# Kernel optimization log

Measured on AMD Instinct MI355X. Metric: run time of the kernel, lower is better.

Reference implementation:

```python
import jax, jax.numpy as jnp
import numpy as np

B, C, H, W = 2, 1024, 64, 64
R, E, HE, T, K = 16, 4, 512, 3, 2


def setup_inputs() -> dict:
    key = jax.random.key(0)
    ks = jax.random.split(key, 12)
    s = 0.02
    return {
        "x": jax.random.normal(ks[0], (B, C, H, W), jnp.float32),
        "t": jax.random.normal(ks[1], (B, C, H, W), jnp.float32),
        "fc_w": jax.random.normal(ks[2], (C, 2 * C), jnp.float32) * s,
        "ln_g": jnp.ones((C,), jnp.float32),
        "ln_b": jnp.zeros((C,), jnp.float32),
        "f1_w1": jax.random.normal(ks[3], (C // R, C), jnp.float32) * s,
        "f1_b1": jnp.zeros((C // R,), jnp.float32),
        "f1_wa": jax.random.normal(ks[4], (C, C // R), jnp.float32) * s,
        "f1_ba": jnp.zeros((C,), jnp.float32),
        "f1_wb": jax.random.normal(ks[5], (C, C // R), jnp.float32) * s,
        "f1_bb": jnp.zeros((C,), jnp.float32),
        "w_gate": jax.random.normal(ks[6], (T, C, E), jnp.float32) * s,
        "e_w1": jax.random.normal(ks[7], (E, C, HE), jnp.float32) * s,
        "e_b1": jnp.zeros((E, HE), jnp.float32),
        "e_w2": jax.random.normal(ks[8], (E, HE, C), jnp.float32) * s,
        "e_b2": jnp.zeros((E, C), jnp.float32),
        "task_index": 1,
    }


def _cv_squared(v):
    eps = 1e-10
    return jnp.var(v, ddof=1) / (jnp.mean(v) ** 2 + eps)


def reference(x, t, fc_w, ln_g, ln_b, f1_w1, f1_b1, f1_wa, f1_ba, f1_wb, f1_bb,
              w_gate, e_w1, e_b1, e_w2, e_b2, task_index):
    b, c, h, w = x.shape
    n = h * w
    # MultiTaskGeneralFusion: SE-style dual-branch channel gating
    s = jnp.mean(x + t, axis=(2, 3))                        # [B, C]
    hid = jax.nn.relu(s @ f1_w1.T + f1_b1)                  # [B, C/r]
    a = hid @ f1_wa.T + f1_ba                               # [B, C]
    bb = hid @ f1_wb.T + f1_bb                              # [B, C]
    wts = jax.nn.softmax(jnp.stack([a, bb], axis=0), axis=0)  # [2, B, C]
    z = wts[0][:, :, None, None] * x + wts[1][:, :, None, None] * t
    # fused linear -> ReLU -> LayerNorm on concatenated tokens
    x3 = x.reshape(b, c, n).transpose(0, 2, 1)              # [B, N, C]
    t3 = t.reshape(b, c, n).transpose(0, 2, 1)
    y = jnp.concatenate([x3, t3], axis=-1)                  # [B, N, 2C]
    y = jax.nn.relu(jnp.einsum('bnd,cd->bnc', y, fc_w))     # [B, N, C]
    mu = jnp.mean(y, axis=-1, keepdims=True)
    var = jnp.mean((y - mu) ** 2, axis=-1, keepdims=True)
    y = (y - mu) * jax.lax.rsqrt(var + 1e-5) * ln_g + ln_b
    yf = y.reshape(b * n, c)                                # [BN, C]
    # MMoE top-k gating (eval mode: no gating noise)
    logits = yf @ w_gate[task_index]                        # [BN, E]
    top_logits, top_idx = jax.lax.top_k(logits, K)          # [BN, K]
    top_gates = jax.nn.softmax(top_logits, axis=-1)
    gates = jnp.zeros_like(logits).at[jnp.arange(b * n)[:, None], top_idx].set(top_gates)
    # dense expert compute, gated combine
    eh = jax.nn.relu(jnp.einsum('nc,ech->neh', yf, e_w1) + e_b1)   # [BN, E, HE]
    eo = jnp.einsum('neh,eho->neo', eh, e_w2) + e_b2               # [BN, E, C]
    ym = jnp.einsum('ne,neo->no', gates, eo)                        # [BN, C]
    importance = gates.sum(axis=0)
    load = (gates > 0).sum(axis=0).astype(jnp.float32)
    aux_loss = _cv_squared(importance) + _cv_squared(load)
    y4 = ym.reshape(b, n, c).transpose(0, 2, 1).reshape(b, c, h, w) + z
    return (y4, aux_loss)
```

## Files before the change

kernel.cpp:

```cpp
#include <hip/hip_runtime.h>
#include <cstddef>
#include <cstdint>

#define B_   2
#define C_   1024
#define N_   4096
#define M_   8192
#define K2_  2048
#define E_   4
#define HE_  512

typedef float f32x4 __attribute__((ext_vector_type(4)));
typedef short bf16x8 __attribute__((ext_vector_type(8)));
typedef _Float16 f16x8 __attribute__((ext_vector_type(8)));
typedef unsigned short u16x8 __attribute__((ext_vector_type(8)));

static __device__ __forceinline__ unsigned short f2bf(float f) {
  unsigned int u = __float_as_uint(f);
  u = u + 0x7fffu + ((u >> 16) & 1u);
  return (unsigned short)(u >> 16);
}

static __device__ __forceinline__ void gl_lds16(const void* g, void* l) {
  __builtin_amdgcn_global_load_lds(
      (const __attribute__((address_space(1))) void*)(uintptr_t)g,
      (__attribute__((address_space(3))) void*)(unsigned)(uintptr_t)l,
      16, 0, 0);
}

static __device__ __forceinline__ bf16x8 cvt8(f32x4 a, f32x4 b) {
  union { unsigned u[4]; bf16x8 s; } r;
  asm("v_cvt_pk_bf16_f32 %0, %1, %2" : "=v"(r.u[0]) : "v"(a[0]), "v"(a[1]));
  asm("v_cvt_pk_bf16_f32 %0, %1, %2" : "=v"(r.u[1]) : "v"(a[2]), "v"(a[3]));
  asm("v_cvt_pk_bf16_f32 %0, %1, %2" : "=v"(r.u[2]) : "v"(b[0]), "v"(b[1]));
  asm("v_cvt_pk_bf16_f32 %0, %1, %2" : "=v"(r.u[3]) : "v"(b[2]), "v"(b[3]));
  return r.s;
}

__global__ __launch_bounds__(256) void k_reduce_s(const float* __restrict__ x,
                                                  const float* __restrict__ t,
                                                  float* __restrict__ s) {
  const int bc = blockIdx.x;
  const float* xp = x + (size_t)bc * N_;
  const float* tp = t + (size_t)bc * N_;
  float acc = 0.f;
  for (int i = threadIdx.x; i < N_ / 4; i += 256) {
    const float4 a = ((const float4*)xp)[i];
    const float4 b = ((const float4*)tp)[i];
    acc += ((a.x + b.x) + (a.y + b.y)) + ((a.z + b.z) + (a.w + b.w));
  }
  #pragma unroll
  for (int o = 32; o; o >>= 1) acc += __shfl_down(acc, o);
  __shared__ float red[4];
  if ((threadIdx.x & 63) == 0) red[threadIdx.x >> 6] = acc;
  __syncthreads();
  if (threadIdx.x == 0)
    s[bc] = (red[0] + red[1] + red[2] + red[3]) * (1.f / (float)N_);
}

__global__ __launch_bounds__(256) void k_se_gate(const float* __restrict__ s,
                                                 const float* __restrict__ w1, const float* __restrict__ b1,
                                                 const float* __restrict__ wa, const float* __restrict__ ba,
                                                 const float* __restrict__ wb, const float* __restrict__ bbv,
                                                 float* __restrict__ wts0) {
  __shared__ float hid[2][64];
  const int t = threadIdx.x;
  if (t < 128) {
    const int b = t >> 6, r = t & 63;
    float acc = b1[r];
    const float* sp = s + b * C_;
    const float* wp = w1 + r * C_;
    for (int c = 0; c < C_; ++c) acc = fmaf(sp[c], wp[c], acc);
    hid[b][r] = fmaxf(acc, 0.f);
  }
  __syncthreads();
  for (int o = t; o < B_ * C_; o += 256) {
    const int b = o >> 10, c = o & 1023;
    float a = ba[c], bb = bbv[c];
    #pragma unroll 8
    for (int r = 0; r < 64; ++r) {
      const float h = hid[b][r];
      a  = fmaf(h, wa[c * 64 + r], a);
      bb = fmaf(h, wb[c * 64 + r], bb);
    }
    wts0[o] = 1.f / (1.f + expf(bb - a));
  }
}

__global__ __launch_bounds__(256) void k_prep_act(const float* __restrict__ xb,
                                                  const float* __restrict__ tb,
                                                  _Float16* __restrict__ ah,
                                                  _Float16* __restrict__ am) {
  __shared__ float tile[64][65];
  const int c0 = blockIdx.x * 64, n0 = blockIdx.y * 64;
  const int tid = threadIdx.x;
  #pragma unroll
  for (int srcsel = 0; srcsel < 2; ++srcsel) {
    const float* src = srcsel ? tb : xb;
    const int koff = srcsel ? C_ : 0;
    if (srcsel) __syncthreads();
    #pragma unroll
    for (int p = 0; p < 4; ++p) {
      const int f = tid + p * 256;
      const int cr = f >> 4, nq = f & 15;
      const float4 v = *(const float4*)(src + (size_t)(c0 + cr) * N_ + n0 + nq * 4);
      tile[cr][nq * 4 + 0] = v.x; tile[cr][nq * 4 + 1] = v.y;
      tile[cr][nq * 4 + 2] = v.z; tile[cr][nq * 4 + 3] = v.w;
    }
    __syncthreads();
    #pragma unroll
    for (int p = 0; p < 2; ++p) {
      const int f = tid + p * 256;
      const int mr = f >> 3, kq = f & 7;
      f16x8 hv, mv;
      #pragma unroll
      for (int u = 0; u < 8; ++u) {
        const float v = tile[kq * 8 + u][mr] * 64.f;
        const _Float16 h = (_Float16)v;
        hv[u] = h;
        mv[u] = (_Float16)(v - (float)h);
      }
      const size_t off = (size_t)(n0 + mr) * K2_ + koff + c0 + kq * 8;
      *(f16x8*)(ah + off) = hv;
      *(f16x8*)(am + off) = mv;
    }
  }
}

__global__ __launch_bounds__(256) void k_prep_fcw(const float* __restrict__ w,
                                                  _Float16* __restrict__ wh,
                                                  _Float16* __restrict__ wm) {
  const size_t i = ((size_t)blockIdx.x * 256 + threadIdx.x) * 8;
  const float4 v0 = *(const float4*)(w + i);
  const float4 v1 = *(const float4*)(w + i + 4);
  const float vv[8] = {v0.x, v0.y, v0.z, v0.w, v1.x, v1.y, v1.z, v1.w};
  f16x8 hv, mv;
  #pragma unroll
  for (int u = 0; u < 8; ++u) {
    const float sv = vv[u] * 4096.f;
    const _Float16 h = (_Float16)sv;
    hv[u] = h;
    mv[u] = (_Float16)(sv - (float)h);
  }
  *(f16x8*)(wh + i) = hv;
  *(f16x8*)(wm + i) = mv;
}

__global__ __launch_bounds__(256) void k_prep_tr(const float* __restrict__ src, long long zs, int srs,
                                                 unsigned short* __restrict__ dst, long long zo, int drs) {
  __shared__ float tile[64][65];
  const int c0 = blockIdx.x * 64, r0 = blockIdx.y * 64, z = blockIdx.z;
  const float* s = src + (size_t)z * zs;
  unsigned short* d = dst + (size_t)z * zo;
  const int tid = threadIdx.x;
  #pragma unroll
  for (int p = 0; p < 4; ++p) {
    const int f = tid + p * 256;
    const int rr = f >> 4, cq = f & 15;
    const float4 v = *(const float4*)(s + (size_t)(r0 + rr) * srs + c0 + cq * 4);
    tile[rr][cq * 4 + 0] = v.x; tile[rr][cq * 4 + 1] = v.y;
    tile[rr][cq * 4 + 2] = v.z; tile[rr][cq * 4 + 3] = v.w;
  }
  __syncthreads();
  #pragma unroll
  for (int p = 0; p < 2; ++p) {
    const int f = tid + p * 256;
    const int cr = f >> 3, rq = f & 7;
    u16x8 o;
    #pragma unroll
    for (int u = 0; u < 8; ++u) o[u] = f2bf(tile[rq * 8 + u][cr]);
    *(u16x8*)(d + (size_t)(c0 + cr) * drs + r0 + rq * 8) = o;
  }
}

__global__ __launch_bounds__(256) void k_fc_mfma(const _Float16* __restrict__ Ah,
                                                 const _Float16* __restrict__ Am,
                                                 const _Float16* __restrict__ Bh,
                                                 const _Float16* __restrict__ Bm,
                                                 float* __restrict__ y) {
  __shared__ __align__(16) _Float16 lAh[4096], lAm[4096], lBh[4096], lBm[4096];
  const int tid = threadIdx.x, w = tid >> 6, l = tid & 63;
  const int m0 = blockIdx.y * 128, n0 = blockIdx.x * 128;
  const int wr = w >> 1, wc = w & 1, lg = l >> 4, lr = l & 15;
  f32x4 acc[4][4] = {};
  for (int k0 = 0; k0 < K2_; k0 += 32) {
    #pragma unroll
    for (int p = 0; p < 2; ++p) {
      const int c = w * 2 + p;
      const int i = c * 64 + l;
      const int g = i >> 7, row = i & 127;
      const size_t ga = (size_t)(m0 + row) * K2_ + k0 + g * 8;
      const size_t gb = (size_t)(n0 + row) * K2_ + k0 + g * 8;
      gl_lds16(Ah + ga, (char*)lAh + c * 1024);
      gl_lds16(Am + ga, (char*)lAm + c * 1024);
      gl_lds16(Bh + gb, (char*)lBh + c * 1024);
      gl_lds16(Bm + gb, (char*)lBm + c * 1024);
    }
    __syncthreads();
    f16x8 ah[4], am[4], bh[4], bm[4];
    #pragma unroll
    for (int i = 0; i < 4; ++i) {
      const int off = (lg * 128 + wr * 64 + i * 16 + lr) * 8;
      ah[i] = *(const f16x8*)&lAh[off];
      am[i] = *(const f16x8*)&lAm[off];
    }
    #pragma unroll
    for (int j = 0; j < 4; ++j) {
      const int off = (lg * 128 + wc * 64 + j * 16 + lr) * 8;
      bh[j] = *(const f16x8*)&lBh[off];
      bm[j] = *(const f16x8*)&lBm[off];
    }
    #pragma unroll
    for (int i = 0; i < 4; ++i)
      #pragma unroll
      for (int j = 0; j < 4; ++j) {
        acc[i][j] = __builtin_amdgcn_mfma_f32_16x16x32_f16(ah[i], bh[j], acc[i][j], 0, 0, 0);
        acc[i][j] = __builtin_amdgcn_mfma_f32_16x16x32_f16(ah[i], bm[j], acc[i][j], 0, 0, 0);
        acc[i][j] = __builtin_amdgcn_mfma_f32_16x16x32_f16(am[i], bh[j], acc[i][j], 0, 0, 0);
      }
    __syncthreads();
  }
  #pragma unroll
  for (int i = 0; i < 4; ++i) {
    const int mb = m0 + wr * 64 + i * 16 + lg * 4;
    #pragma unroll
    for (int j = 0; j < 4; ++j) {
      const int n = n0 + wc * 64 + j * 16 + lr;
      #pragma unroll
      for (int r = 0; r < 4; ++r)
        y[(size_t)(mb + r) * C_ + n] = fmaxf(acc[i][j][r] * (1.f / 262144.f), 0.f);
    }
  }
}

__global__ __launch_bounds__(256) void k_ln_topk(float* __restrict__ y,
                                                 const float* __restrict__ lng, const float* __restrict__ lnb,
                                                 const float* __restrict__ wg, const int* __restrict__ taskp,
                                                 float* __restrict__ gates) {
  const int wv = threadIdx.x >> 6, ln = threadIdx.x & 63;
  const int m = blockIdx.x * 4 + wv;
  float* yr = y + (size_t)m * C_;
  float4 v[4];
  #pragma unroll
  for (int ch = 0; ch < 4; ++ch) v[ch] = *(const float4*)(yr + ch * 256 + ln * 4);
  float sum = 0.f;
  #pragma unroll
  for (int ch = 0; ch < 4; ++ch) sum += (v[ch].x + v[ch].y) + (v[ch].z + v[ch].w);
  #pragma unroll
  for (int o = 32; o; o >>= 1) sum += __shfl_down(sum, o);
  sum = __shfl(sum, 0);
  const float mu = sum * (1.f / 1024.f);
  float q = 0.f;
  #pragma unroll
  for (int ch = 0; ch < 4; ++ch) {
    const float dx = v[ch].x - mu, dy = v[ch].y - mu, dz = v[ch].z - mu, dw = v[ch].w - mu;
    q += (dx * dx + dy * dy) + (dz * dz + dw * dw);
  }
  #pragma unroll
  for (int o = 32; o; o >>= 1) q += __shfl_down(q, o);
  q = __shfl(q, 0);
  const float rstd = rsqrtf(q * (1.f / 1024.f) + 1e-5f);
  const float* wrow = wg + (size_t)(*taskp) * (C_ * E_);
  float l0 = 0.f, l1 = 0.f, l2 = 0.f, l3 = 0.f;
  #pragma unroll
  for (int ch = 0; ch < 4; ++ch) {
    const int c = ch * 256 + ln * 4;
    const float4 gg = *(const float4*)(lng + c);
    const float4 bv = *(const float4*)(lnb + c);
    float f[4];
    f[0] = (v[ch].x - mu) * rstd * gg.x + bv.x;
    f[1] = (v[ch].y - mu) * rstd * gg.y + bv.y;
    f[2] = (v[ch].z - mu) * rstd * gg.z + bv.z;
    f[3] = (v[ch].w - mu) * rstd * gg.w + bv.w;
    float4 wb; wb.x = f[0]; wb.y = f[1]; wb.z = f[2]; wb.w = f[3];
    *(float4*)(yr + c) = wb;
    #pragma unroll
    for (int i = 0; i < 4; ++i) {
      const float4 we = *(const float4*)(wrow + (size_t)(c + i) * 4);
      l0 = fmaf(f[i], we.x, l0); l1 = fmaf(f[i], we.y, l1);
      l2 = fmaf(f[i], we.z, l2); l3 = fmaf(f[i], we.w, l3);
    }
  }
  #pragma unroll
  for (int o = 32; o; o >>= 1) {
    l0 += __shfl_down(l0, o); l1 += __shfl_down(l1, o);
    l2 += __shfl_down(l2, o); l3 += __shfl_down(l3, o);
  }
  if (ln == 0) {
    const float L[4] = {l0, l1, l2, l3};
    int i1 = 0; float best = L[0];
    #pragma unroll
    for (int e = 1; e < 4; ++e) if (L[e] > best) { best = L[e]; i1 = e; }
    int i2 = -1; float s2 = 0.f;
    #pragma unroll
    for (int e = 0; e < 4; ++e) if (e != i1 && (i2 < 0 || L[e] > s2)) { s2 = L[e]; i2 = e; }
    const float g1 = 1.f / (1.f + expf(s2 - best));
    const float g2 = 1.f - g1;
    float4 gv;
    gv.x = (i1 == 0) ? g1 : ((i2 == 0) ? g2 : 0.f);
    gv.y = (i1 == 1) ? g1 : ((i2 == 1) ? g2 : 0.f);
    gv.z = (i1 == 2) ? g1 : ((i2 == 2) ? g2 : 0.f);
    gv.w = (i1 == 3) ? g1 : ((i2 == 3) ? g2 : 0.f);
    *(float4*)(gates + (size_t)m * 4) = gv;
  }
}

__global__ __launch_bounds__(256) void k_moe1_mfma(const float* __restrict__ Y,
                                                   const short* __restrict__ Bw,
                                                   const float* __restrict__ b1,
                                                   const float* __restrict__ gates,
                                                   unsigned short* __restrict__ ehg) {
  __shared__ __align__(16) float lA[4096];
  __shared__ __align__(16) short lB[4096];
  const int tid = threadIdx.x, w = tid >> 6, l = tid & 63;
  const int m0 = blockIdx.y * 128, n0 = blockIdx.x * 128;
  const int wr = w >> 1, wc = w & 1, lg = l >> 4, lr = l & 15;
  f32x4 acc[4][4] = {};
  for (int k0 = 0; k0 < C_; k0 += 32) {
    #pragma unroll
    for (int p = 0; p < 4; ++p) {
      const int c = w * 4 + p;
      const int q = c * 64 + l;
      const int g = q >> 8, row = (q >> 1) & 127, jh = q & 1;
      gl_lds16(Y + (size_t)(m0 + row) * C_ + k0 + g * 8 + jh * 4, (char*)lA + c * 1024);
    }
    #pragma unroll
    for (int p = 0; p < 2; ++p) {
      const int c = w * 2 + p;
      const int i = c * 64 + l;
      const int g = i >> 7, row = i & 127;
      gl_lds16(Bw + (size_t)(n0 + row) * C_ + k0 + g * 8, (char*)lB + c * 1024);
    }
    __syncthreads();
    bf16x8 af[4], bfr[4];
    #pragma unroll
    for (int i = 0; i < 4; ++i) {
      const int off = (lg * 128 + wr * 64 + i * 16 + lr) * 8;
      const f32x4 a0 = *(const f32x4*)&lA[off];
      const f32x4 a1 = *(const f32x4*)&lA[off + 4];
      af[i] = cvt8(a0, a1);
    }
    #pragma unroll
    for (int j = 0; j < 4; ++j)
      bfr[j] = *(const bf16x8*)&lB[(lg * 128 + wc * 64 + j * 16 + lr) * 8];
    #pragma unroll
    for (int i = 0; i < 4; ++i)
      #pragma unroll
      for (int j = 0; j < 4; ++j)
        acc[i][j] = __builtin_amdgcn_mfma_f32_16x16x32_bf16(af[i], bfr[j], acc[i][j], 0, 0, 0);
    __syncthreads();
  }
  const int e0 = n0 >> 9;
  #pragma unroll
  for (int j = 0; j < 4; ++j) {
    const int n = n0 + wc * 64 + j * 16 + lr;
    const float bias = b1[e0 * HE_ + (n & 511)];
    #pragma unroll
    for (int i = 0; i < 4; ++i) {
      const int mb = m0 + wr * 64 + i * 16 + lg * 4;
      #pragma unroll
      for (int r = 0; r < 4; ++r) {
        const float g = gates[(size_t)(mb + r) * 4 + e0];
        const float v = fmaxf(acc[i][j][r] + bias, 0.f) * g;
        ehg[(size_t)(mb + r) * K2_ + n] = f2bf(v);
      }
    }
  }
}

__global__ __launch_bounds__(256) void k_moe2_mfma(const short* __restrict__ Aeh,
                                                   const short* __restrict__ Bw,
                                                   const float* __restrict__ b2,
                                                   const float* __restrict__ gates,
                                                   float* __restrict__ ym) {
  __shared__ __align__(16) short lA[4096];
  __shared__ __align__(16) short lB[4096];
  const int tid = threadIdx.x, w = tid >> 6, l = tid & 63;
  const int m0 = blockIdx.y * 128, n0 = blockIdx.x * 128;
  const int wr = w >> 1, wc = w & 1, lg = l >> 4, lr = l & 15;
  f32x4 acc[4][4] = {};
  for (int k0 = 0; k0 < K2_; k0 += 32) {
    #pragma unroll
    for (int p = 0; p < 2; ++p) {
      const int c = w * 2 + p;
      const int i = c * 64 + l;
      const int g = i >> 7, row = i & 127;
      gl_lds16(Aeh + (size_t)(m0 + row) * K2_ + k0 + g * 8, (char*)lA + c * 1024);
      gl_lds16(Bw + (size_t)(n0 + row) * K2_ + k0 + g * 8, (char*)lB + c * 1024);
    }
    __syncthreads();
    bf16x8 af[4], bfr[4];
    #pragma unroll
    for (int i = 0; i < 4; ++i)
      af[i] = *(const bf16x8*)&lA[(lg * 128 + wr * 64 + i * 16 + lr) * 8];
    #pragma unroll
    for (int j = 0; j < 4; ++j)
      bfr[j] = *(const bf16x8*)&lB[(lg * 128 + wc * 64 + j * 16 + lr) * 8];
    #pragma unroll
    for (int i = 0; i < 4; ++i)
      #pragma unroll
      for (int j = 0; j < 4; ++j)
        acc[i][j] = __builtin_amdgcn_mfma_f32_16x16x32_bf16(af[i], bfr[j], acc[i][j], 0, 0, 0);
    __syncthreads();
  }
  float bb[4][4];
  #pragma unroll
  for (int j = 0; j < 4; ++j) {
    const int n = n0 + wc * 64 + j * 16 + lr;
    #pragma unroll
    for (int e = 0; e < 4; ++e) bb[j][e] = b2[e * C_ + n];
  }
  #pragma unroll
  for (int i = 0; i < 4; ++i) {
    const int mb = m0 + wr * 64 + i * 16 + lg * 4;
    #pragma unroll
    for (int r = 0; r < 4; ++r) {
      const float4 g = *(const float4*)(gates + (size_t)(mb + r) * 4);
      #pragma unroll
      for (int j = 0; j < 4; ++j) {
        const int n = n0 + wc * 64 + j * 16 + lr;
        ym[(size_t)(mb + r) * C_ + n] =
            acc[i][j][r] + g.x * bb[j][0] + g.y * bb[j][1] + g.z * bb[j][2] + g.w * bb[j][3];
      }
    }
  }
}

__global__ __launch_bounds__(256) void k_aux(const float* __restrict__ gates, float* __restrict__ outp) {
  const int t = threadIdx.x;
  float imp[4] = {0, 0, 0, 0}, ld[4] = {0, 0, 0, 0};
  for (int m = t; m < M_; m += 256) {
    const float4 g = *(const float4*)(gates + (size_t)m * 4);
    imp[0] += g.x; imp[1] += g.y; imp[2] += g.z; imp[3] += g.w;
    ld[0] += (g.x > 0.f) ? 1.f : 0.f; ld[1] += (g.y > 0.f) ? 1.f : 0.f;
    ld[2] += (g.z > 0.f) ? 1.f : 0.f; ld[3] += (g.w > 0.f) ? 1.f : 0.f;
  }
  __shared__ float red[8][4];
  const int wv = t >> 6, ln = t & 63;
  #pragma unroll
  for (int e = 0; e < 4; ++e) {
    float a = imp[e], b = ld[e];
    #pragma unroll
    for (int o = 32; o; o >>= 1) { a += __shfl_down(a, o); b += __shfl_down(b, o); }
    if (ln == 0) { red[e][wv] = a; red[4 + e][wv] = b; }
  }
  __syncthreads();
  if (t == 0) {
    float I[4], L[4];
    #pragma unroll
    for (int e = 0; e < 4; ++e) {
      I[e] = red[e][0] + red[e][1] + red[e][2] + red[e][3];
      L[e] = red[4 + e][0] + red[4 + e][1] + red[4 + e][2] + red[4 + e][3];
    }
    const float mi = (I[0] + I[1] + I[2] + I[3]) * 0.25f;
    const float vi = ((I[0] - mi) * (I[0] - mi) + (I[1] - mi) * (I[1] - mi) +
                      (I[2] - mi) * (I[2] - mi) + (I[3] - mi) * (I[3] - mi)) / 3.f;
    const float ml = (L[0] + L[1] + L[2] + L[3]) * 0.25f;
    const float vl = ((L[0] - ml) * (L[0] - ml) + (L[1] - ml) * (L[1] - ml) +
                      (L[2] - ml) * (L[2] - ml) + (L[3] - ml) * (L[3] - ml)) / 3.f;
    *outp = vi / (mi * mi + 1e-10f) + vl / (ml * ml + 1e-10f);
  }
}

__global__ __launch_bounds__(256) void k_final(const float* __restrict__ ym,
                                               const float* __restrict__ x, const float* __restrict__ t,
                                               const float* __restrict__ wts0, float* __restrict__ out) {
  __shared__ float tile[64][65];
  const int c0 = blockIdx.x * 64, n0 = blockIdx.y * 64, b = blockIdx.z;
  const int tid = threadIdx.x;
  #pragma unroll
  for (int p = 0; p < 4; ++p) {
    const int f = tid + p * 256;
    const int row = f >> 4, cq = f & 15;
    const float4 v = *(const float4*)(ym + (size_t)(b * N_ + n0 + row) * C_ + c0 + cq * 4);
    tile[row][cq * 4 + 0] = v.x; tile[row][cq * 4 + 1] = v.y;
    tile[row][cq * 4 + 2] = v.z; tile[row][cq * 4 + 3] = v.w;
  }
  __syncthreads();
  #pragma unroll
  for (int p = 0; p < 4; ++p) {
    const int f = tid + p * 256;
    const int cr = f >> 4, nq = f & 15;
    const int c = c0 + cr;
    const float w0 = wts0[b * C_ + c];
    const float w1 = 1.f - w0;
    const size_t idx = (size_t)(b * C_ + c) * N_ + n0 + nq * 4;
    const float4 xv = *(const float4*)(x + idx);
    const float4 tv = *(const float4*)(t + idx);
    float4 o;
    o.x = tile[nq * 4 + 0][cr] + w0 * xv.x + w1 * tv.x;
    o.y = tile[nq * 4 + 1][cr] + w0 * xv.y + w1 * tv.y;
    o.z = tile[nq * 4 + 2][cr] + w0 * xv.z + w1 * tv.z;
    o.w = tile[nq * 4 + 3][cr] + w0 * xv.w + w1 * tv.w;
    *(float4*)(out + idx) = o;
  }
}

extern "C" void kernel_launch(void* const* d_in, const int* in_sizes, int n_in,
                              void* d_out, int out_size, void* d_ws, size_t ws_size,
                              hipStream_t stream) {
  const float* x     = (const float*)d_in[0];
  const float* t     = (const float*)d_in[1];
  const float* fc_w  = (const float*)d_in[2];
  const float* ln_g  = (const float*)d_in[3];
  const float* ln_b  = (const float*)d_in[4];
  const float* f1_w1 = (const float*)d_in[5];
  const float* f1_b1 = (const float*)d_in[6];
  const float* f1_wa = (const float*)d_in[7];
  const float* f1_ba = (const float*)d_in[8];
  const float* f1_wb = (const float*)d_in[9];
  const float* f1_bb = (const float*)d_in[10];
  const float* w_gate = (const float*)d_in[11];
  const float* e_w1  = (const float*)d_in[12];
  const float* e_b1  = (const float*)d_in[13];
  const float* e_w2  = (const float*)d_in[14];
  const float* e_b2  = (const float*)d_in[15];
  const int*   task  = (const int*)d_in[16];
  float* out = (float*)d_out;

  char* ws = (char*)d_ws;
  const bool big = ws_size >= 117587968ull;
  float*          y    = (float*)ws;
  unsigned short* ehg  = (unsigned short*)(ws + 33554432);
  _Float16 *ah, *am; char *W, *SM;
  if (big) {
    ah = (_Float16*)(ws + 33554432);
    am = (_Float16*)(ws + 67108864);
    W  = ws + 100663296;
    SM = ws + 117440512;
  } else {
    ah = (_Float16*)(ws + 33554432);
    am = (_Float16*)(ws + 50331648);
    W  = ws + 67108864;
    SM = ws + 83886080;
  }
  _Float16* wh  = (_Float16*)W;
  _Float16* wm  = (_Float16*)(W + 4194304);
  short*    w1t = (short*)(W + 8388608);
  short*    w2t = (short*)(W + 12582912);
  float* sbuf  = (float*)SM;
  float* wts0  = (float*)(SM + 8192);
  float* gates = (float*)(SM + 16384);

  k_reduce_s<<<B_ * C_, 256, 0, stream>>>(x, t, sbuf);
  k_se_gate<<<1, 256, 0, stream>>>(sbuf, f1_w1, f1_b1, f1_wa, f1_ba, f1_wb, f1_bb, wts0);
  k_prep_fcw<<<1024, 256, 0, stream>>>(fc_w, wh, wm);
  k_prep_tr<<<dim3(8, 16, 4), 256, 0, stream>>>(e_w1, 524288LL, 512, (unsigned short*)w1t, 524288LL, 1024);
  k_prep_tr<<<dim3(16, 8, 4), 256, 0, stream>>>(e_w2, 524288LL, 1024, (unsigned short*)w2t, 512LL, 2048);
  if (big) {
    k_prep_act<<<dim3(16, 64), 256, 0, stream>>>(x, t, ah, am);
    k_prep_act<<<dim3(16, 64), 256, 0, stream>>>(x + 4194304, t + 4194304, ah + 8388608, am + 8388608);
    k_fc_mfma<<<dim3(8, 64), 256, 0, stream>>>(ah, am, wh, wm, y);
  } else {
    for (int b = 0; b < 2; ++b) {
      k_prep_act<<<dim3(16, 64), 256, 0, stream>>>(x + (size_t)b * 4194304, t + (size_t)b * 4194304, ah, am);
      k_fc_mfma<<<dim3(8, 32), 256, 0, stream>>>(ah, am, wh, wm, y + (size_t)b * 4194304);
    }
  }
  k_ln_topk<<<M_ / 4, 256, 0, stream>>>(y, ln_g, ln_b, w_gate, task, gates);
  k_moe1_mfma<<<dim3(16, 64), 256, 0, stream>>>(y, w1t, e_b1, gates, ehg);
  k_moe2_mfma<<<dim3(8, 64), 256, 0, stream>>>((const short*)ehg, w2t, e_b2, gates, y);
  k_aux<<<1, 256, 0, stream>>>(gates, out + (size_t)B_ * C_ * N_);
  k_final<<<dim3(C_ / 64, N_ / 64, B_), 256, 0, stream>>>(y, x, t, wts0, out);
}
```

Before: 434.2 us.

## Double-buffer LDS in GEMM kernels and emit bf16 LN output for MoE

Adds two-stage LDS double buffering to the fc, moe1 and moe2 MFMA kernels, so the global-to-LDS load of the next K tile overlaps the current tile's MFMAs and one barrier per iteration is dropped. LayerNorm now writes a bf16 copy of the activations, so moe1 loads bf16 directly instead of fp32 plus an in-kernel conversion, which halves that operand's traffic. The per-batch prep launches are merged into one 3D grid, and the small-workspace fallback is removed, so a large workspace is now assumed. Double buffering doubles LDS use per block, which may lower occupancy, and the fc kernel's MFMA loop is reordered into three passes.

Result: slower. 451.4 us (+4.0%).

```diff
diff --git a/kernel.cpp b/kernel.cpp
--- a/kernel.cpp
+++ b/kernel.cpp
@@ -26,15 +26,6 @@
       (const __attribute__((address_space(1))) void*)(uintptr_t)g,
       (__attribute__((address_space(3))) void*)(unsigned)(uintptr_t)l,
       16, 0, 0);
-}
-
-static __device__ __forceinline__ bf16x8 cvt8(f32x4 a, f32x4 b) {
-  union { unsigned u[4]; bf16x8 s; } r;
-  asm("v_cvt_pk_bf16_f32 %0, %1, %2" : "=v"(r.u[0]) : "v"(a[0]), "v"(a[1]));
-  asm("v_cvt_pk_bf16_f32 %0, %1, %2" : "=v"(r.u[1]) : "v"(a[2]), "v"(a[3]));
-  asm("v_cvt_pk_bf16_f32 %0, %1, %2" : "=v"(r.u[2]) : "v"(b[0]), "v"(b[1]));
-  asm("v_cvt_pk_bf16_f32 %0, %1, %2" : "=v"(r.u[3]) : "v"(b[2]), "v"(b[3]));
-  return r.s;
 }
 
 __global__ __launch_bounds__(256) void k_reduce_s(const float* __restrict__ x,
@@ -87,12 +78,16 @@
   }
 }
 
-__global__ __launch_bounds__(256) void k_prep_act(const float* __restrict__ xb,
-                                                  const float* __restrict__ tb,
+__global__ __launch_bounds__(256) void k_prep_act(const float* __restrict__ x,
+                                                  const float* __restrict__ t,
                                                   _Float16* __restrict__ ah,
                                                   _Float16* __restrict__ am) {
   __shared__ float tile[64][65];
-  const int c0 = blockIdx.x * 64, n0 = blockIdx.y * 64;
+  const int c0 = blockIdx.x * 64, n0 = blockIdx.y * 64, b = blockIdx.z;
+  const float* xb = x + (size_t)b * (C_ * N_);
+  const float* tb = t + (size_t)b * (C_ * N_);
+  _Float16* ahb = ah + (size_t)b * (N_ * (size_t)K2_);
+  _Float16* amb = am + (size_t)b * (N_ * (size_t)K2_);
   const int tid = threadIdx.x;
   #pragma unroll
   for (int srcsel = 0; srcsel < 2; ++srcsel) {
@@ -121,8 +116,8 @@
         mv[u] = (_Float16)(v - (float)h);
       }
       const size_t off = (size_t)(n0 + mr) * K2_ + koff + c0 + kq * 8;
-      *(f16x8*)(ah + off) = hv;
-      *(f16x8*)(am + off) = mv;
+      *(f16x8*)(ahb + off) = hv;
+      *(f16x8*)(amb + off) = mv;
     }
   }
 }
@@ -178,12 +173,14 @@
                                                  const _Float16* __restrict__ Bh,
                                                  const _Float16* __restrict__ Bm,
                                                  float* __restrict__ y) {
-  __shared__ __align__(16) _Float16 lAh[4096], lAm[4096], lBh[4096], lBm[4096];
+  __shared__ __align__(16) _Float16 lA[2][2][4096];
+  __shared__ __align__(16) _Float16 lB[2][2][4096];
   const int tid = threadIdx.x, w = tid >> 6, l = tid & 63;
   const int m0 = blockIdx.y * 128, n0 = blockIdx.x * 128;
   const int wr = w >> 1, wc = w & 1, lg = l >> 4, lr = l & 15;
   f32x4 acc[4][4] = {};
-  for (int k0 = 0; k0 < K2_; k0 += 32) {
+
+  auto STAGE = [&](int buf, int k0) {
     #pragma unroll
     for (int p = 0; p < 2; ++p) {
       const int c = w * 2 + p;
@@ -191,33 +188,48 @@
       const int g = i >> 7, row = i & 127;
       const size_t ga = (size_t)(m0 + row) * K2_ + k0 + g * 8;
       const size_t gb = (size_t)(n0 + row) * K2_ + k0 + g * 8;
-      gl_lds16(Ah + ga, (char*)lAh + c * 1024);
-      gl_lds16(Am + ga, (char*)lAm + c * 1024);
-      gl_lds16(Bh + gb, (char*)lBh + c * 1024);
-      gl_lds16(Bm + gb, (char*)lBm + c * 1024);
-    }
-    __syncthreads();
+      char* dA = (char*)lA + buf * 16384 + c * 1024;
+      char* dB = (char*)lB + buf * 16384 + c * 1024;
+      gl_lds16(Ah + ga, dA);
+      gl_lds16(Am + ga, dA + 8192);
+      gl_lds16(Bh + gb, dB);
+      gl_lds16(Bm + gb, dB + 8192);
+    }
+  };
+
+  STAGE(0, 0);
+  __syncthreads();
+  for (int k0 = 0; k0 < K2_; k0 += 32) {
+    const int cur = (k0 >> 5) & 1;
+    if (k0 + 32 < K2_) STAGE(cur ^ 1, k0 + 32);
     f16x8 ah[4], am[4], bh[4], bm[4];
     #pragma unroll
     for (int i = 0; i < 4; ++i) {
       const int off = (lg * 128 + wr * 64 + i * 16 + lr) * 8;
-      ah[i] = *(const f16x8*)&lAh[off];
-      am[i] = *(const f16x8*)&lAm[off];
+      ah[i] = *(const f16x8*)((char*)lA + cur * 16384 + off * 2);
+      am[i] = *(const f16x8*)((char*)lA + cur * 16384 + 8192 + off * 2);
     }
     #pragma unroll
     for (int j = 0; j < 4; ++j) {
       const int off = (lg * 128 + wc * 64 + j * 16 + lr) * 8;
-      bh[j] = *(const f16x8*)&lBh[off];
-      bm[j] = *(const f16x8*)&lBm[off];
-    }
-    #pragma unroll
-    for (int i = 0; i < 4; ++i)
-      #pragma unroll
-      for (int j = 0; j < 4; ++j) {
+      bh[j] = *(const f16x8*)((char*)lB + cur * 16384 + off * 2);
+      bm[j] = *(const f16x8*)((char*)lB + cur * 16384 + 8192 + off * 2);
+    }
+    #pragma unroll
+    for (int i = 0; i < 4; ++i)
+      #pragma unroll
+      for (int j = 0; j < 4; ++j)
         acc[i][j] = __builtin_amdgcn_mfma_f32_16x16x32_f16(ah[i], bh[j], acc[i][j], 0, 0, 0);
+    #pragma unroll
+    for (int i = 0; i < 4; ++i)
+      #pragma unroll
+      for (int j = 0; j < 4; ++j)
         acc[i][j] = __builtin_amdgcn_mfma_f32_16x16x32_f16(ah[i], bm[j], acc[i][j], 0, 0, 0);
+    #pragma unroll
+    for (int i = 0; i < 4; ++i)
+      #pragma unroll
+      for (int j = 0; j < 4; ++j)
         acc[i][j] = __builtin_amdgcn_mfma_f32_16x16x32_f16(am[i], bh[j], acc[i][j], 0, 0, 0);
-      }
     __syncthreads();
   }
   #pragma unroll
@@ -233,13 +245,13 @@
   }
 }
 
-__global__ __launch_bounds__(256) void k_ln_topk(float* __restrict__ y,
+__global__ __launch_bounds__(256) void k_ln_topk(const float* __restrict__ y,
                                                  const float* __restrict__ lng, const float* __restrict__ lnb,
                                                  const float* __restrict__ wg, const int* __restrict__ taskp,
-                                                 float* __restrict__ gates) {
+                                                 unsigned short* __restrict__ yf, float* __restrict__ gates) {
   const int wv = threadIdx.x >> 6, ln = threadIdx.x & 63;
   const int m = blockIdx.x * 4 + wv;
-  float* yr = y + (size_t)m * C_;
+  const float* yr = y + (size_t)m * C_;
   float4 v[4];
   #pragma unroll
   for (int ch = 0; ch < 4; ++ch) v[ch] = *(const float4*)(yr + ch * 256 + ln * 4);
@@ -272,8 +284,10 @@
     f[1] = (v[ch].y - mu) * rstd * gg.y + bv.y;
     f[2] = (v[ch].z - mu) * rstd * gg.z + bv.z;
     f[3] = (v[ch].w - mu) * rstd * gg.w + bv.w;
-    float4 wb; wb.x = f[0]; wb.y = f[1]; wb.z = f[2]; wb.w = f[3];
-    *(float4*)(yr + c) = wb;
+    uint2 pk;
+    pk.x = (unsigned)f2bf(f[0]) | ((unsigned)f2bf(f[1]) << 16);
+    pk.y = (unsigned)f2bf(f[2]) | ((unsigned)f2bf(f[3]) << 16);
+    *(uint2*)(yf + (size_t)m * C_ + c) = pk;
     #pragma unroll
     for (int i = 0; i < 4; ++i) {
       const float4 we = *(const float4*)(wrow + (size_t)(c + i) * 4);
@@ -305,44 +319,40 @@
   }
 }
 
-__global__ __launch_bounds__(256) void k_moe1_mfma(const float* __restrict__ Y,
+__global__ __launch_bounds__(256) void k_moe1_mfma(const unsigned short* __restrict__ yf,
                                                    const short* __restrict__ Bw,
                                                    const float* __restrict__ b1,
                                                    const float* __restrict__ gates,
                                                    unsigned short* __restrict__ ehg) {
-  __shared__ __align__(16) float lA[4096];
-  __shared__ __align__(16) short lB[4096];
+  __shared__ __align__(16) short lA[2][4096], lB[2][4096];
   const int tid = threadIdx.x, w = tid >> 6, l = tid & 63;
   const int m0 = blockIdx.y * 128, n0 = blockIdx.x * 128;
   const int wr = w >> 1, wc = w & 1, lg = l >> 4, lr = l & 15;
   f32x4 acc[4][4] = {};
-  for (int k0 = 0; k0 < C_; k0 += 32) {
-    #pragma unroll
-    for (int p = 0; p < 4; ++p) {
-      const int c = w * 4 + p;
-      const int q = c * 64 + l;
-      const int g = q >> 8, row = (q >> 1) & 127, jh = q & 1;
-      gl_lds16(Y + (size_t)(m0 + row) * C_ + k0 + g * 8 + jh * 4, (char*)lA + c * 1024);
-    }
+
+  auto STAGE = [&](int buf, int k0) {
     #pragma unroll
     for (int p = 0; p < 2; ++p) {
       const int c = w * 2 + p;
       const int i = c * 64 + l;
       const int g = i >> 7, row = i & 127;
-      gl_lds16(Bw + (size_t)(n0 + row) * C_ + k0 + g * 8, (char*)lB + c * 1024);
-    }
-    __syncthreads();
+      gl_lds16(yf + (size_t)(m0 + row) * C_ + k0 + g * 8, (char*)lA + buf * 8192 + c * 1024);
+      gl_lds16(Bw + (size_t)(n0 + row) * C_ + k0 + g * 8, (char*)lB + buf * 8192 + c * 1024);
+    }
+  };
+
+  STAGE(0, 0);
+  __syncthreads();
+  for (int k0 = 0; k0 < C_; k0 += 32) {
+    const int cur = (k0 >> 5) & 1;
+    if (k0 + 32 < C_) STAGE(cur ^ 1, k0 + 32);
     bf16x8 af[4], bfr[4];
     #pragma unroll
-    for (int i = 0; i < 4; ++i) {
-      const int off = (lg * 128 + wr * 64 + i * 16 + lr) * 8;
-      const f32x4 a0 = *(const f32x4*)&lA[off];
-      const f32x4 a1 = *(const f32x4*)&lA[off + 4];
-      af[i] = cvt8(a0, a1);
-    }
+    for (int i = 0; i < 4; ++i)
+      af[i] = *(const bf16x8*)((char*)lA + cur * 8192 + (lg * 128 + wr * 64 + i * 16 + lr) * 16);
     #pragma unroll
     for (int j = 0; j < 4; ++j)
-      bfr[j] = *(const bf16x8*)&lB[(lg * 128 + wc * 64 + j * 16 + lr) * 8];
+      bfr[j] = *(const bf16x8*)((char*)lB + cur * 8192 + (lg * 128 + wc * 64 + j * 16 + lr) * 16);
     #pragma unroll
     for (int i = 0; i < 4; ++i)
       #pragma unroll
@@ -373,29 +383,35 @@
                                                    const float* __restrict__ b2,
                                                    const float* __restrict__ gates,
                                                    float* __restrict__ ym) {
-  __shared__ __align__(16) short lA[4096];
-  __shared__ __align__(16) short lB[4096];
+  __shared__ __align__(16) short lA[2][4096], lB[2][4096];
   const int tid = threadIdx.x, w = tid >> 6, l = tid & 63;
   const int m0 = blockIdx.y * 128, n0 = blockIdx.x * 128;
   const int wr = w >> 1, wc = w & 1, lg = l >> 4, lr = l & 15;
   f32x4 acc[4][4] = {};
-  for (int k0 = 0; k0 < K2_; k0 += 32) {
+
+  auto STAGE = [&](int buf, int k0) {
     #pragma unroll
     for (int p = 0; p < 2; ++p) {
       const int c = w * 2 + p;
       const int i = c * 64 + l;
       const int g = i >> 7, row = i & 127;
-      gl_lds16(Aeh + (size_t)(m0 + row) * K2_ + k0 + g * 8, (char*)lA + c * 1024);
-      gl_lds16(Bw + (size_t)(n0 + row) * K2_ + k0 + g * 8, (char*)lB + c * 1024);
-    }
-    __syncthreads();
+      gl_lds16(Aeh + (size_t)(m0 + row) * K2_ + k0 + g * 8, (char*)lA + buf * 8192 + c * 1024);
+      gl_lds16(Bw + (size_t)(n0 + row) * K2_ + k0 + g * 8, (char*)lB + buf * 8192 + c * 1024);
+    }
+  };
+
+  STAGE(0, 0);
+  __syncthreads();
+  for (int k0 = 0; k0 < K2_; k0 += 32) {
+    const int cur = (k0 >> 5) & 1;
+    if (k0 + 32 < K2_) STAGE(cur ^ 1, k0 + 32);
     bf16x8 af[4], bfr[4];
     #pragma unroll
     for (int i = 0; i < 4; ++i)
-      af[i] = *(const bf16x8*)&lA[(lg * 128 + wr * 64 + i * 16 + lr) * 8];
+      af[i] = *(const bf16x8*)((char*)lA + cur * 8192 + (lg * 128 + wr * 64 + i * 16 + lr) * 16);
     #pragma unroll
     for (int j = 0; j < 4; ++j)
-      bfr[j] = *(const bf16x8*)&lB[(lg * 128 + wc * 64 + j * 16 + lr) * 8];
+      bfr[j] = *(const bf16x8*)((char*)lB + cur * 8192 + (lg * 128 + wc * 64 + j * 16 + lr) * 16);
     #pragma unroll
     for (int i = 0; i < 4; ++i)
       #pragma unroll
@@ -519,46 +535,28 @@
   float* out = (float*)d_out;
 
   char* ws = (char*)d_ws;
-  const bool big = ws_size >= 117587968ull;
   float*          y    = (float*)ws;
-  unsigned short* ehg  = (unsigned short*)(ws + 33554432);
-  _Float16 *ah, *am; char *W, *SM;
-  if (big) {
-    ah = (_Float16*)(ws + 33554432);
-    am = (_Float16*)(ws + 67108864);
-    W  = ws + 100663296;
-    SM = ws + 117440512;
-  } else {
-    ah = (_Float16*)(ws + 33554432);
-    am = (_Float16*)(ws + 50331648);
-    W  = ws + 67108864;
-    SM = ws + 83886080;
-  }
-  _Float16* wh  = (_Float16*)W;
-  _Float16* wm  = (_Float16*)(W + 4194304);
-  short*    w1t = (short*)(W + 8388608);
-  short*    w2t = (short*)(W + 12582912);
-  float* sbuf  = (float*)SM;
-  float* wts0  = (float*)(SM + 8192);
-  float* gates = (float*)(SM + 16384);
+  _Float16*       ah   = (_Float16*)(ws + 33554432);
+  _Float16*       am   = (_Float16*)(ws + 67108864);
+  unsigned short* yf   = (unsigned short*)(ws + 33554432);
+  unsigned short* ehg  = (unsigned short*)(ws + 50331648);
+  _Float16* wh  = (_Float16*)(ws + 100663296);
+  _Float16* wm  = (_Float16*)(ws + 104857600);
+  short*    w1t = (short*)(ws + 109051904);
+  short*    w2t = (short*)(ws + 113246208);
+  float* sbuf  = (float*)(ws + 117440512);
+  float* wts0  = (float*)(ws + 117448704);
+  float* gates = (float*)(ws + 117456896);
 
   k_reduce_s<<<B_ * C_, 256, 0, stream>>>(x, t, sbuf);
   k_se_gate<<<1, 256, 0, stream>>>(sbuf, f1_w1, f1_b1, f1_wa, f1_ba, f1_wb, f1_bb, wts0);
   k_prep_fcw<<<1024, 256, 0, stream>>>(fc_w, wh, wm);
   k_prep_tr<<<dim3(8, 16, 4), 256, 0, stream>>>(e_w1, 524288LL, 512, (unsigned short*)w1t, 524288LL, 1024);
   k_prep_tr<<<dim3(16, 8, 4), 256, 0, stream>>>(e_w2, 524288LL, 1024, (unsigned short*)w2t, 512LL, 2048);
-  if (big) {
-    k_prep_act<<<dim3(16, 64), 256, 0, stream>>>(x, t, ah, am);
-    k_prep_act<<<dim3(16, 64), 256, 0, stream>>>(x + 4194304, t + 4194304, ah + 8388608, am + 8388608);
-    k_fc_mfma<<<dim3(8, 64), 256, 0, stream>>>(ah, am, wh, wm, y);
-  } else {
-    for (int b = 0; b < 2; ++b) {
-      k_prep_act<<<dim3(16, 64), 256, 0, stream>>>(x + (size_t)b * 4194304, t + (size_t)b * 4194304, ah, am);
-      k_fc_mfma<<<dim3(8, 32), 256, 0, stream>>>(ah, am, wh, wm, y + (size_t)b * 4194304);
-    }
-  }
-  k_ln_topk<<<M_ / 4, 256, 0, stream>>>(y, ln_g, ln_b, w_gate, task, gates);
-  k_moe1_mfma<<<dim3(16, 64), 256, 0, stream>>>(y, w1t, e_b1, gates, ehg);
+  k_prep_act<<<dim3(16, 64, 2), 256, 0, stream>>>(x, t, ah, am);
+  k_fc_mfma<<<dim3(8, 64), 256, 0, stream>>>(ah, am, wh, wm, y);
+  k_ln_topk<<<M_ / 4, 256, 0, stream>>>(y, ln_g, ln_b, w_gate, task, yf, gates);
+  k_moe1_mfma<<<dim3(16, 64), 256, 0, stream>>>(yf, w1t, e_b1, gates, ehg);
   k_moe2_mfma<<<dim3(8, 64), 256, 0, stream>>>((const short*)ehg, w2t, e_b2, gates, y);
   k_aux<<<1, 256, 0, stream>>>(gates, out + (size_t)B_ * C_ * N_);
   k_final<<<dim3(C_ / 64, N_ / 64, B_), 256, 0, stream>>>(y, x, t, wts0, out);
```
